# Optimization experiments

Measured on AMD Instinct MI355X. Metric: run time of the kernel, lower is better.

The kernel has to match this reference:

```python
import jax, jax.numpy as jnp
import numpy as np

HID = 512
VOCAB = 64
SAMPLE_PROB = 0.1


def lstm_cell(x, h, c, w_ih, w_hh, b_ih, b_hh):
    # PyTorch LSTMCell: gates ordered (i, f, g, o)
    gates = x @ w_ih.T + b_ih + h @ w_hh.T + b_hh
    i, f, g, o = jnp.split(gates, 4, axis=-1)
    i = jax.nn.sigmoid(i)
    f = jax.nn.sigmoid(f)
    g = jnp.tanh(g)
    o = jax.nn.sigmoid(o)
    c_new = f * c + i * g
    h_new = o * jnp.tanh(c_new)
    return h_new, c_new


def _linear_params(key, out_dim, in_dim):
    bound = 1.0 / np.sqrt(in_dim)
    kw, kb = jax.random.split(key)
    w = jax.random.uniform(kw, (out_dim, in_dim), jnp.float32, -bound, bound)
    b = jax.random.uniform(kb, (out_dim,), jnp.float32, -bound, bound)
    return w, b


def setup_inputs() -> dict:
    key = jax.random.key(0)
    ks = jax.random.split(key, 9)
    B, R, T = 128, 512, 128
    phi_w, phi_b = _linear_params(ks[0], HID, HID)          # decoder -> context
    psi_w, psi_b = _linear_params(ks[1], HID, HID)          # listener -> context
    w_ih0, b_ih0 = _linear_params(ks[2], 4 * HID, HID + VOCAB)
    w_hh0, b_hh0 = _linear_params(ks[3], 4 * HID, HID)
    w_ih1, b_ih1 = _linear_params(ks[4], 4 * HID, HID)
    w_hh1, b_hh1 = _linear_params(ks[5], 4 * HID, HID)
    out_w, out_b = _linear_params(ks[6], VOCAB, HID)
    h = jax.random.normal(ks[7], (B, R, HID), jnp.float32)
    y = jax.random.randint(ks[8], (B, T + 1), 0, VOCAB)
    return dict(h=h, phi_w=phi_w, phi_b=phi_b, psi_w=psi_w, psi_b=psi_b,
                w_ih0=w_ih0, w_hh0=w_hh0, b_ih0=b_ih0, b_hh0=b_hh0,
                w_ih1=w_ih1, w_hh1=w_hh1, b_ih1=b_ih1, b_hh1=b_hh1,
                out_w=out_w, out_b=out_b, y=y)


def reference(h, phi_w, phi_b, psi_w, psi_b,
              w_ih0, w_hh0, b_ih0, b_hh0,
              w_ih1, w_hh1, b_ih1, b_hh1,
              out_w, out_b, y):
    B = h.shape[0]
    T = y.shape[1] - 1
    # psi is applied to h identically every step; hoist it out of the loop.
    hp = h @ psi_w.T + psi_b                     # [B, R, HID]
    keys = jax.random.split(jax.random.key(42), T)
    z0 = y[:, 0]
    zeros = jnp.zeros((B, HID), h.dtype)
    carry0 = (zeros, zeros, zeros, zeros, z0)    # s0, cs0, s1, cs1, z

    def step(carry, xs):
        s0, cs0, s1, cs1, z = carry
        key, y_next = xs
        z_oh = jax.nn.one_hot(z, VOCAB, dtype=h.dtype)
        # additive-style attention context
        sq = s1 @ phi_w.T + phi_b                # [B, HID]
        e = jnp.einsum('bd,brd->br', sq, hp)     # [B, R]
        alpha = jax.nn.softmax(e, axis=1)
        c = jnp.einsum('br,brd->bd', alpha, hp)  # [B, HID]
        inp = jnp.concatenate([z_oh, c], axis=1)
        s0, cs0 = lstm_cell(inp, s0, cs0, w_ih0, w_hh0, b_ih0, b_hh0)
        s1, cs1 = lstm_cell(s0, s1, cs1, w_ih1, w_hh1, b_ih1, b_hh1)
        o = s1 @ out_w.T + out_b                 # [B, VOCAB]
        k1, k2 = jax.random.split(key)
        sampled = jax.random.categorical(k1, o, axis=1)
        do_sample = jax.random.bernoulli(k2, SAMPLE_PROB, (B,))
        z_next = jnp.where(do_sample, sampled, y_next)
        return (s0, cs0, s1, cs1, z_next), o

    xs = (keys, y[:, 1:].T)                      # per-step key, teacher token [T, B]
    _, outs = jax.lax.scan(step, carry0, xs)     # outs: [T, B, VOCAB]
    return jnp.transpose(outs, (1, 0, 2))        # [B, T, VOCAB]
```

## Files before the change

kernel.cpp:

```cpp
#include <hip/hip_runtime.h>
#include <math.h>


#define JAX_PARTITIONABLE 1

#define B_   128
#define HID_ 512
#define VOC_ 64
#define T_   128

#define S0_OFF    0u
#define CS0_OFF   65536u
#define S1_OFF    131072u
#define CS1_OFF   196608u
#define SQT_OFF   262144u
#define CPR_OFF   327680u
#define AMAT_OFF  393216u
#define W1PSI_OFF 655360u
#define BIAS0_OFF 1703936u
#define V_OFF     1705984u
#define PART_OFF  1706496u
#define GUM_OFF   5900800u
#define UB_OFF    6949376u
#define Z_OFF     6965760u

#define TF_TINY 1.17549435e-38f

__device__ __forceinline__ void tf2x32(unsigned k0, unsigned k1,
                                       unsigned& x0, unsigned& x1) {
  unsigned ks2 = k0 ^ k1 ^ 0x1BD11BDAu;
  const unsigned ks[3] = {k0, k1, ks2};
  const int rot0[4] = {13, 15, 26, 6};
  const int rot1[4] = {17, 29, 16, 24};
  x0 += ks[0]; x1 += ks[1];
  #pragma unroll
  for (int i = 0; i < 5; ++i) {
    #pragma unroll
    for (int r = 0; r < 4; ++r) {
      int rr = (i & 1) ? rot1[r] : rot0[r];
      x0 += x1;
      x1 = (x1 << rr) | (x1 >> (32 - rr));
      x1 ^= x0;
    }
    x0 += ks[(i + 1) % 3];
    x1 += ks[(i + 2) % 3] + (unsigned)(i + 1);
  }
}

__device__ __forceinline__ float bits_to_unit(unsigned bits) {
  return __uint_as_float((bits >> 9) | 0x3f800000u) - 1.0f;
}

__global__ __launch_bounds__(256) void k_random(const int* __restrict__ y,
                                                float* __restrict__ gum,
                                                float* __restrict__ ub,
                                                int* __restrict__ z) {
  int t = blockIdx.x, tid = threadIdx.x;
  unsigned ka, kb, k1a, k1b, k2a, k2b;
#if JAX_PARTITIONABLE
  ka = 0u; kb = (unsigned)t;
  tf2x32(0u, 42u, ka, kb);
  k1a = 0u; k1b = 0u; tf2x32(ka, kb, k1a, k1b);
  k2a = 0u; k2b = 1u; tf2x32(ka, kb, k2a, k2b);
  for (int j = tid; j < B_ * VOC_; j += 256) {
    unsigned x0 = 0u, x1 = (unsigned)j;
    tf2x32(k1a, k1b, x0, x1);
    unsigned bits = x0 ^ x1;
    float f = bits_to_unit(bits);
    float u = fmaxf(TF_TINY, f * (1.0f - TF_TINY) + TF_TINY);
    gum[(size_t)t * (B_ * VOC_) + j] = -logf(-logf(u));
  }
  if (tid < B_) {
    unsigned x0 = 0u, x1 = (unsigned)tid;
    tf2x32(k2a, k2b, x0, x1);
    ub[t * B_ + tid] = bits_to_unit(x0 ^ x1);
  }
#else
  {
    unsigned x0, x1, y0, y1;
    if (t < 64) {
      x0 = 2u * t;     x1 = 128u + 2u * t;     tf2x32(0u, 42u, x0, x1); ka = x0;
      y0 = 2u * t + 1; y1 = 128u + 2u * t + 1; tf2x32(0u, 42u, y0, y1); kb = y0;
    } else {
      x0 = 2u * t - 128u; x1 = 2u * t;         tf2x32(0u, 42u, x0, x1); ka = x1;
      y0 = 2u * t - 127u; y1 = 2u * t + 1;     tf2x32(0u, 42u, y0, y1); kb = y1;
    }
    unsigned e0a = 0u, e0b = 2u; tf2x32(ka, kb, e0a, e0b);
    unsigned e1a = 1u, e1b = 3u; tf2x32(ka, kb, e1a, e1b);
    k1a = e0a; k1b = e1a; k2a = e0b; k2b = e1b;
  }
  for (int j = tid; j < B_ * VOC_; j += 256) {
    unsigned x0, x1, bits;
    if (j < 4096) { x0 = (unsigned)j; x1 = (unsigned)(4096 + j); tf2x32(k1a, k1b, x0, x1); bits = x0; }
    else          { x0 = (unsigned)(j - 4096); x1 = (unsigned)j; tf2x32(k1a, k1b, x0, x1); bits = x1; }
    float f = bits_to_unit(bits);
    float u = fmaxf(TF_TINY, f * (1.0f - TF_TINY) + TF_TINY);
    gum[(size_t)t * (B_ * VOC_) + j] = -logf(-logf(u));
  }
  if (tid < B_) {
    unsigned x0, x1, bits;
    if (tid < 64) { x0 = (unsigned)tid; x1 = (unsigned)(64 + tid); tf2x32(k2a, k2b, x0, x1); bits = x0; }
    else          { x0 = (unsigned)(tid - 64); x1 = (unsigned)tid; tf2x32(k2a, k2b, x0, x1); bits = x1; }
    ub[t * B_ + tid] = bits_to_unit(bits);
  }
#endif
  if (t == 0 && tid < B_) z[tid] = y[tid * (T_ + 1)];
}

__global__ __launch_bounds__(256) void k_fold_misc(
    const float* __restrict__ psi_w, const float* __restrict__ phi_b,
    const float* __restrict__ w_ih0, const float* __restrict__ psi_b,
    const float* __restrict__ b_ih0, const float* __restrict__ b_hh0,
    float* __restrict__ vvec, float* __restrict__ bias0) {
  int gid = blockIdx.x * 256 + threadIdx.x;
  if (gid < 512) {
    float acc = 0.f;
    for (int j = 0; j < 512; ++j) acc += psi_w[j * 512 + gid] * phi_b[j];
    vvec[gid] = acc;
  } else if (gid < 512 + 2048) {
    int j = gid - 512;
    float acc = b_ih0[j] + b_hh0[j];
    const float* wr = w_ih0 + (size_t)j * 576 + 64;
    for (int d = 0; d < 512; ++d) acc += wr[d] * psi_b[d];
    bias0[j] = acc;
  }
}

__global__ __launch_bounds__(256) void k_gemm_tn(
    const float* __restrict__ A, const float* __restrict__ B, float* __restrict__ C,
    int K, int lda, int ldb, int ldc) {
  __shared__ float As[32][33], Bs[32][33];
  int n0 = blockIdx.x * 32, m0 = blockIdx.y * 32;
  int t = threadIdx.x, tx = t & 31, ty = t >> 5;
  float acc[4] = {0.f, 0.f, 0.f, 0.f};
  for (int k0 = 0; k0 < K; k0 += 32) {
    for (int l = t; l < 1024; l += 256) {
      int jj = l >> 5, mm = l & 31;
      As[jj][mm] = A[(size_t)(k0 + jj) * lda + m0 + mm];
      Bs[jj][mm] = B[(size_t)(k0 + jj) * ldb + n0 + mm];
    }
    __syncthreads();
    #pragma unroll 8
    for (int jj = 0; jj < 32; ++jj) {
      float bv = Bs[jj][tx];
      #pragma unroll
      for (int q = 0; q < 4; ++q) acc[q] += As[jj][ty + 8 * q] * bv;
    }
    __syncthreads();
  }
  #pragma unroll
  for (int q = 0; q < 4; ++q) C[(size_t)(m0 + ty + 8 * q) * ldc + n0 + tx] = acc[q];
}

__global__ __launch_bounds__(256) void k_gemm_nn(
    const float* __restrict__ A, const float* __restrict__ B, float* __restrict__ C,
    int K, int lda, int aoff, int ldb, int ldc) {
  __shared__ float As[32][33], Bs[32][33];
  int n0 = blockIdx.x * 32, m0 = blockIdx.y * 32;
  int t = threadIdx.x, tx = t & 31, ty = t >> 5;
  float acc[4] = {0.f, 0.f, 0.f, 0.f};
  for (int k0 = 0; k0 < K; k0 += 32) {
    for (int l = t; l < 1024; l += 256) {
      int r = l >> 5, c = l & 31;
      As[c][r] = A[(size_t)(m0 + r) * lda + aoff + k0 + c];
      Bs[r][c] = B[(size_t)(k0 + r) * ldb + n0 + c];
    }
    __syncthreads();
    #pragma unroll 8
    for (int kk = 0; kk < 32; ++kk) {
      float bv = Bs[kk][tx];
      #pragma unroll
      for (int q = 0; q < 4; ++q) acc[q] += As[kk][ty + 8 * q] * bv;
    }
    __syncthreads();
  }
  #pragma unroll
  for (int q = 0; q < 4; ++q) C[(size_t)(m0 + ty + 8 * q) * ldc + n0 + tx] = acc[q];
}

__global__ __launch_bounds__(256) void k_sqt_init(const float* __restrict__ vvec,
                                                  float* __restrict__ sqt) {
  int lin = blockIdx.x * 256 + threadIdx.x;
  if (lin < B_ * HID_) sqt[lin] = vvec[lin & 511];
}

__global__ __launch_bounds__(256) void k_attn(const float* __restrict__ h,
                                              const float* __restrict__ sqt,
                                              float* __restrict__ cpr) {
  __shared__ float hs[16 * 512];
  __shared__ float es[16];
  __shared__ float ps[16];
  int b = blockIdx.x, t = threadIdx.x;
  const float* hb = h + (size_t)b * 512 * 512;
  const float* sq = sqt + b * 512;
  int krow = t >> 4, g = t & 15;
  float m = -INFINITY, l = 0.f, a0 = 0.f, a1 = 0.f;
  int d0 = t, d1 = t + 256;
  for (int r0 = 0; r0 < 512; r0 += 16) {
    __syncthreads();
    const float* hr = hb + (size_t)(r0 + krow) * 512;
    float ep = 0.f;
    #pragma unroll
    for (int i = 0; i < 8; ++i) {
      int d = i * 64 + g * 4;
      float4 hv = *(const float4*)(hr + d);
      float4 sv = *(const float4*)(sq + d);
      ep += hv.x * sv.x + hv.y * sv.y + hv.z * sv.z + hv.w * sv.w;
      *(float4*)(&hs[krow * 512 + d]) = hv;
    }
    ep += __shfl_xor(ep, 1);
    ep += __shfl_xor(ep, 2);
    ep += __shfl_xor(ep, 4);
    ep += __shfl_xor(ep, 8);
    if (g == 0) es[krow] = ep;
    __syncthreads();
    float mc = es[0];
    #pragma unroll
    for (int k = 1; k < 16; ++k) mc = fmaxf(mc, es[k]);
    float mn = fmaxf(m, mc);
    if (t < 16) ps[t] = expf(es[t] - mn);
    __syncthreads();
    float sc = expf(m - mn);
    float ls = 0.f;
    float n0 = a0 * sc, n1 = a1 * sc;
    #pragma unroll
    for (int k = 0; k < 16; ++k) {
      float p = ps[k];
      ls += p;
      n0 += p * hs[k * 512 + d0];
      n1 += p * hs[k * 512 + d1];
    }
    m = mn; l = l * sc + ls; a0 = n0; a1 = n1;
  }
  cpr[b * 512 + d0] = a0 / l;
  cpr[b * 512 + d1] = a1 / l;
}

__global__ __launch_bounds__(256) void k_lstm_gemm(
    const float* __restrict__ X0, const float* __restrict__ W0,
    const float* __restrict__ X1, const float* __restrict__ W1,
    float* __restrict__ part) {
  __shared__ float Xs[16][128];
  __shared__ float Ws[16][64];
  int t = threadIdx.x;
  int jt = blockIdx.x * 64;
  int s = blockIdx.y;
  const float* X; const float* W; int kbase;
  if (s < 8) { X = X0; W = W0; kbase = s * 64; }
  else       { X = X1; W = W1; kbase = (s - 8) * 64; }
  float acc[8][4];
  #pragma unroll
  for (int i = 0; i < 8; ++i)
    #pragma unroll
    for (int q = 0; q < 4; ++q) acc[i][q] = 0.f;
  int b0 = (t & 15) * 8, j0 = (t >> 4) * 4;
  for (int kk = 0; kk < 64; kk += 16) {
    #pragma unroll
    for (int lo = 0; lo < 3; ++lo) {
      int u = t + lo * 256;
      if (u < 512) {
        int row = u >> 2;
        int kq = (u & 3) * 4;
        float4 xv = *(const float4*)(X + (size_t)row * 512 + kbase + kk + kq);
        Xs[kq + 0][row] = xv.x; Xs[kq + 1][row] = xv.y;
        Xs[kq + 2][row] = xv.z; Xs[kq + 3][row] = xv.w;
      } else {
        int w = u - 512;
        int row = w >> 2;
        int kq = (w & 3) * 4;
        float4 wv = *(const float4*)(W + (size_t)(jt + row) * 512 + kbase + kk + kq);
        Ws[kq + 0][row] = wv.x; Ws[kq + 1][row] = wv.y;
        Ws[kq + 2][row] = wv.z; Ws[kq + 3][row] = wv.w;
      }
    }
    __syncthreads();
    #pragma unroll
    for (int k = 0; k < 16; ++k) {
      float4 xa = *(const float4*)&Xs[k][b0];
      float4 xb = *(const float4*)&Xs[k][b0 + 4];
      float4 wa = *(const float4*)&Ws[k][j0];
      float xr[8] = {xa.x, xa.y, xa.z, xa.w, xb.x, xb.y, xb.z, xb.w};
      float wr[4] = {wa.x, wa.y, wa.z, wa.w};
      #pragma unroll
      for (int i = 0; i < 8; ++i)
        #pragma unroll
        for (int q = 0; q < 4; ++q) acc[i][q] += xr[i] * wr[q];
    }
    __syncthreads();
  }
  #pragma unroll
  for (int i = 0; i < 8; ++i) {
    float* pr = part + ((size_t)(s * 128 + b0 + i)) * 2048 + jt + j0;
    *(float4*)pr = make_float4(acc[i][0], acc[i][1], acc[i][2], acc[i][3]);
  }
}

__device__ __forceinline__ float sigm(float x) { return 1.0f / (1.0f + expf(-x)); }

__global__ __launch_bounds__(256) void k_lstm_cell(
    const float* __restrict__ part, const float* __restrict__ biasA,
    const float* __restrict__ bi, const float* __restrict__ bh,
    const float* __restrict__ woh, int ldoh,
    const int* __restrict__ z, float* __restrict__ s, float* __restrict__ cs) {
  int lin = blockIdx.x * 256 + threadIdx.x;
  int b = lin >> 9, d = lin & 511;
  int zb = woh ? z[b] : 0;
  float g4[4];
  #pragma unroll
  for (int g = 0; g < 4; ++g) {
    int j = g * 512 + d;
    float sum = biasA ? biasA[j] : (bi[j] + bh[j]);
    if (woh) sum += woh[(size_t)j * ldoh + zb];
    #pragma unroll
    for (int sl = 0; sl < 16; ++sl)
      sum += part[((size_t)(sl * 128 + b)) * 2048 + j];
    g4[g] = sum;
  }
  float ig = sigm(g4[0]), fg = sigm(g4[1]);
  float gg = tanhf(g4[2]), og = sigm(g4[3]);
  float cn = fg * cs[lin] + ig * gg;
  float sn = og * tanhf(cn);
  cs[lin] = cn;
  s[lin] = sn;
}

__global__ __launch_bounds__(512) void k_tail(
    int t, const float* __restrict__ part,
    const float* __restrict__ bi, const float* __restrict__ bh,
    const float* __restrict__ outw, const float* __restrict__ outb,
    const float* __restrict__ AmatT, const float* __restrict__ vvec,
    const float* __restrict__ gum, const float* __restrict__ ub,
    const int* __restrict__ y, const float* __restrict__ h,
    float* __restrict__ out, float* __restrict__ s1g, float* __restrict__ cs1,
    int* __restrict__ z, float* __restrict__ cpr) {
  __shared__ __align__(16) float hs[64 * 512];
  __shared__ __align__(16) float sl[512];
  __shared__ __align__(16) float sq[512];
  __shared__ float red[256];
  __shared__ float es_l[64];
  int b = blockIdx.x, tid = threadIdx.x;

  {
    int d = tid;
    int lin = b * 512 + d;
    float g4[4];
    #pragma unroll
    for (int g = 0; g < 4; ++g) {
      int j = g * 512 + d;
      float sum = bi[j] + bh[j];
      #pragma unroll
      for (int slc = 0; slc < 16; ++slc)
        sum += part[((size_t)(slc * 128 + b)) * 2048 + j];
      g4[g] = sum;
    }
    float ig = sigm(g4[0]), fg = sigm(g4[1]);
    float gg = tanhf(g4[2]), og = sigm(g4[3]);
    float cn = fg * cs1[lin] + ig * gg;
    float sn = og * tanhf(cn);
    cs1[lin] = cn;
    s1g[lin] = sn;
    sl[d] = sn;
  }
  __syncthreads();

  if (tid < 256) {
    int v = tid & 63, kg = tid >> 6;
    const float* wr = outw + (size_t)v * 512 + kg * 128;
    const float* sr = sl + kg * 128;
    float sum = 0.f;
    #pragma unroll 8
    for (int k = 0; k < 128; k += 4) {
      float4 w4 = *(const float4*)(wr + k);
      float4 s4 = *(const float4*)(sr + k);
      sum += w4.x * s4.x + w4.y * s4.y + w4.z * s4.z + w4.w * s4.w;
    }
    red[kg * 64 + v] = sum;
  }
  __syncthreads();
  if (tid < 64) {
    float o = red[tid] + red[64 + tid] + red[128 + tid] + red[192 + tid] + outb[tid];
    out[((size_t)b * T_ + t) * VOC_ + tid] = o;
    float val = o + gum[((size_t)t * B_ + b) * VOC_ + tid];
    int idx = tid;
    #pragma unroll
    for (int off = 1; off < 64; off <<= 1) {
      float ov = __shfl_xor(val, off);
      int oi = __shfl_xor(idx, off);
      if (ov > val || (ov == val && oi < idx)) { val = ov; idx = oi; }
    }
    if (tid == 0) {
      float u = ub[t * B_ + b];
      z[b] = (u < 0.1f) ? idx : y[b * (T_ + 1) + t + 1];
    }
  }

  {
    int d = tid;
    float av = vvec[d];
    const float* At = AmatT + d;
    for (int k = 0; k < 512; k += 4) {
      float p0 = At[(size_t)k * 512]       * sl[k];
      float p1 = At[(size_t)(k + 1) * 512] * sl[k + 1];
      float p2 = At[(size_t)(k + 2) * 512] * sl[k + 2];
      float p3 = At[(size_t)(k + 3) * 512] * sl[k + 3];
      av += p0 + p1 + p2 + p3;
    }
    sq[d] = av;
  }
  if (t == T_ - 1) return;
  __syncthreads();

  const float* hb = h + (size_t)b * (512 * 512);
  int krow = tid >> 4;
  int gq = tid & 15;
  int col = gq * 4;
  float4 sqr[8];
  #pragma unroll
  for (int i = 0; i < 8; ++i) sqr[i] = *(const float4*)(&sq[i * 64 + col]);

  float4 hv0[8], hv1[8];
  {
    const float* hr0 = hb + (size_t)krow * 512;
    const float* hr1 = hb + (size_t)(krow + 32) * 512;
    #pragma unroll
    for (int i = 0; i < 8; ++i) {
      hv0[i] = *(const float4*)(hr0 + i * 64 + col);
      hv1[i] = *(const float4*)(hr1 + i * 64 + col);
    }
    float ep0 = 0.f, ep1 = 0.f;
    #pragma unroll
    for (int i = 0; i < 8; ++i) {
      ep0 += hv0[i].x * sqr[i].x + hv0[i].y * sqr[i].y + hv0[i].z * sqr[i].z + hv0[i].w * sqr[i].w;
      *(float4*)(&hs[krow * 512 + i * 64 + col]) = hv0[i];
      ep1 += hv1[i].x * sqr[i].x + hv1[i].y * sqr[i].y + hv1[i].z * sqr[i].z + hv1[i].w * sqr[i].w;
      *(float4*)(&hs[(krow + 32) * 512 + i * 64 + col]) = hv1[i];
    }
    ep0 += __shfl_xor(ep0, 1); ep0 += __shfl_xor(ep0, 2);
    ep0 += __shfl_xor(ep0, 4); ep0 += __shfl_xor(ep0, 8);
    ep1 += __shfl_xor(ep1, 1); ep1 += __shfl_xor(ep1, 2);
    ep1 += __shfl_xor(ep1, 4); ep1 += __shfl_xor(ep1, 8);
    if (gq == 0) { es_l[krow] = ep0; es_l[krow + 32] = ep1; }
  }
  __syncthreads();

  float m = -INFINITY, l = 0.f, a0 = 0.f;
  int d0 = tid;
  int lane15 = tid & 15;
  for (int g = 0; g < 8; ++g) {
    if (g < 7) {
      const float* hr0 = hb + (size_t)((g + 1) * 64 + krow) * 512;
      const float* hr1 = hb + (size_t)((g + 1) * 64 + krow + 32) * 512;
      #pragma unroll
      for (int i = 0; i < 8; ++i) {
        hv0[i] = *(const float4*)(hr0 + i * 64 + col);
        hv1[i] = *(const float4*)(hr1 + i * 64 + col);
      }
    }
    #pragma unroll
    for (int lc = 0; lc < 4; ++lc) {
      float mc = es_l[lc * 16];
      #pragma unroll
      for (int k = 1; k < 16; ++k) mc = fmaxf(mc, es_l[lc * 16 + k]);
      float mn = fmaxf(m, mc);
      float pw = expf(es_l[lc * 16 + lane15] - mn);
      float sc = expf(m - mn);
      float ls = 0.f;
      float n0 = a0 * sc;
      #pragma unroll
      for (int k = 0; k < 16; ++k) {
        float p = __shfl(pw, k);
        ls += p;
        n0 += p * hs[(lc * 16 + k) * 512 + d0];
      }
      m = mn; l = l * sc + ls; a0 = n0;
    }
    __syncthreads();
    if (g < 7) {
      float ep0 = 0.f, ep1 = 0.f;
      #pragma unroll
      for (int i = 0; i < 8; ++i) {
        ep0 += hv0[i].x * sqr[i].x + hv0[i].y * sqr[i].y + hv0[i].z * sqr[i].z + hv0[i].w * sqr[i].w;
        *(float4*)(&hs[krow * 512 + i * 64 + col]) = hv0[i];
        ep1 += hv1[i].x * sqr[i].x + hv1[i].y * sqr[i].y + hv1[i].z * sqr[i].z + hv1[i].w * sqr[i].w;
        *(float4*)(&hs[(krow + 32) * 512 + i * 64 + col]) = hv1[i];
      }
      ep0 += __shfl_xor(ep0, 1); ep0 += __shfl_xor(ep0, 2);
      ep0 += __shfl_xor(ep0, 4); ep0 += __shfl_xor(ep0, 8);
      ep1 += __shfl_xor(ep1, 1); ep1 += __shfl_xor(ep1, 2);
      ep1 += __shfl_xor(ep1, 4); ep1 += __shfl_xor(ep1, 8);
      if (gq == 0) { es_l[krow] = ep0; es_l[krow + 32] = ep1; }
    }
    __syncthreads();
  }
  cpr[b * 512 + d0] = a0 / l;
}

extern "C" void kernel_launch(void* const* d_in, const int* in_sizes, int n_in,
                              void* d_out, int out_size, void* d_ws, size_t ws_size,
                              hipStream_t stream) {
  const float* h     = (const float*)d_in[0];
  const float* phi_w = (const float*)d_in[1];
  const float* phi_b = (const float*)d_in[2];
  const float* psi_w = (const float*)d_in[3];
  const float* psi_b = (const float*)d_in[4];
  const float* w_ih0 = (const float*)d_in[5];
  const float* w_hh0 = (const float*)d_in[6];
  const float* b_ih0 = (const float*)d_in[7];
  const float* b_hh0 = (const float*)d_in[8];
  const float* w_ih1 = (const float*)d_in[9];
  const float* w_hh1 = (const float*)d_in[10];
  const float* b_ih1 = (const float*)d_in[11];
  const float* b_hh1 = (const float*)d_in[12];
  const float* out_w = (const float*)d_in[13];
  const float* out_b = (const float*)d_in[14];
  const int*   y     = (const int*)d_in[15];

  float* out = (float*)d_out;
  float* ws  = (float*)d_ws;

  float* s0    = ws + S0_OFF;
  float* cs0   = ws + CS0_OFF;
  float* s1    = ws + S1_OFF;
  float* cs1   = ws + CS1_OFF;
  float* sqt   = ws + SQT_OFF;
  float* cpr   = ws + CPR_OFF;
  float* AmatT = ws + AMAT_OFF;
  float* W1psi = ws + W1PSI_OFF;
  float* bias0 = ws + BIAS0_OFF;
  float* vvec  = ws + V_OFF;
  float* part  = ws + PART_OFF;
  float* gum   = ws + GUM_OFF;
  float* ub    = ws + UB_OFF;
  int*   z     = (int*)(ws + Z_OFF);

  hipMemsetAsync(s0, 0, 4 * (size_t)B_ * HID_ * sizeof(float), stream);

  k_random<<<T_, 256, 0, stream>>>(y, gum, ub, z);
  k_fold_misc<<<10, 256, 0, stream>>>(psi_w, phi_b, w_ih0, psi_b, b_ih0, b_hh0, vvec, bias0);
  k_gemm_tn<<<dim3(16, 16), 256, 0, stream>>>(phi_w, psi_w, AmatT, 512, 512, 512, 512);
  k_gemm_nn<<<dim3(16, 64), 256, 0, stream>>>(w_ih0, psi_w, W1psi, 512, 576, 64, 512, 512);
  k_sqt_init<<<256, 256, 0, stream>>>(vvec, sqt);
  k_attn<<<128, 256, 0, stream>>>(h, sqt, cpr);

  for (int t = 0; t < T_; ++t) {
    k_lstm_gemm<<<dim3(32, 16), 256, 0, stream>>>(cpr, W1psi, s0, w_hh0, part);
    k_lstm_cell<<<256, 256, 0, stream>>>(part, bias0, nullptr, nullptr, w_ih0, 576, z, s0, cs0);
    k_lstm_gemm<<<dim3(32, 16), 256, 0, stream>>>(s0, w_ih1, s1, w_hh1, part);
    k_tail<<<128, 512, 0, stream>>>(t, part, b_ih1, b_hh1, out_w, out_b, AmatT, vvec,
                                    gum, ub, y, h, out, s1, cs1, z, cpr);
  }
}
```

Measured before the change: 12.72 ms.

## Fuse LSTM gate GEMM with cell update using ping-pong state buffers

Result: slower. 18.46 ms (+45.1%).

```diff
diff --git a/kernel.cpp b/kernel.cpp
--- a/kernel.cpp
+++ b/kernel.cpp
@@ -184,6 +184,15 @@
   if (lin < B_ * HID_) sqt[lin] = vvec[lin & 511];
 }
 
+__global__ __launch_bounds__(256) void k_transpose_ow(const float* __restrict__ outw,
+                                                      float* __restrict__ outwT) {
+  int gid = blockIdx.x * 256 + threadIdx.x;
+  if (gid < 512 * 64) {
+    int k = gid >> 6, v = gid & 63;
+    outwT[gid] = outw[(size_t)v * 512 + k];
+  }
+}
+
 __global__ __launch_bounds__(256) void k_attn(const float* __restrict__ h,
                                               const float* __restrict__ sqt,
                                               float* __restrict__ cpr) {
@@ -236,103 +245,85 @@
   cpr[b * 512 + d1] = a1 / l;
 }
 
-__global__ __launch_bounds__(256) void k_lstm_gemm(
+__device__ __forceinline__ float sigm(float x) { return 1.0f / (1.0f + expf(-x)); }
+
+__global__ __launch_bounds__(256) void k_fused(
     const float* __restrict__ X0, const float* __restrict__ W0,
     const float* __restrict__ X1, const float* __restrict__ W1,
-    float* __restrict__ part) {
-  __shared__ float Xs[16][128];
-  __shared__ float Ws[16][64];
-  int t = threadIdx.x;
-  int jt = blockIdx.x * 64;
-  int s = blockIdx.y;
-  const float* X; const float* W; int kbase;
-  if (s < 8) { X = X0; W = W0; kbase = s * 64; }
-  else       { X = X1; W = W1; kbase = (s - 8) * 64; }
-  float acc[8][4];
+    const float* __restrict__ biasA, const float* __restrict__ bi,
+    const float* __restrict__ bh, const float* __restrict__ woh, int ldoh,
+    const int* __restrict__ z, float* __restrict__ snew, float* __restrict__ cs) {
+  __shared__ float Xs[64][16];
+  __shared__ float Ws[64][64];
+  __shared__ float tot[16][64];
+  int tid = threadIdx.x;
+  int dt0 = blockIdx.x * 16, bt0 = blockIdx.y * 16;
+  int b = tid & 15, j0 = (tid >> 4) * 4;
+  float total[4];
+  int zb = woh ? z[bt0 + b] : 0;
   #pragma unroll
-  for (int i = 0; i < 8; ++i)
-    #pragma unroll
-    for (int q = 0; q < 4; ++q) acc[i][q] = 0.f;
-  int b0 = (t & 15) * 8, j0 = (t >> 4) * 4;
-  for (int kk = 0; kk < 64; kk += 16) {
-    #pragma unroll
-    for (int lo = 0; lo < 3; ++lo) {
-      int u = t + lo * 256;
-      if (u < 512) {
-        int row = u >> 2;
-        int kq = (u & 3) * 4;
-        float4 xv = *(const float4*)(X + (size_t)row * 512 + kbase + kk + kq);
-        Xs[kq + 0][row] = xv.x; Xs[kq + 1][row] = xv.y;
-        Xs[kq + 2][row] = xv.z; Xs[kq + 3][row] = xv.w;
-      } else {
-        int w = u - 512;
-        int row = w >> 2;
-        int kq = (w & 3) * 4;
-        float4 wv = *(const float4*)(W + (size_t)(jt + row) * 512 + kbase + kk + kq);
-        Ws[kq + 0][row] = wv.x; Ws[kq + 1][row] = wv.y;
-        Ws[kq + 2][row] = wv.z; Ws[kq + 3][row] = wv.w;
+  for (int q = 0; q < 4; ++q) {
+    int jl = j0 + q;
+    int jg = (jl >> 4) * 512 + dt0 + (jl & 15);
+    float tq = biasA ? biasA[jg] : (bi[jg] + bh[jg]);
+    if (woh) tq += woh[(size_t)jg * ldoh + zb];
+    total[q] = tq;
+  }
+  for (int s = 0; s < 16; ++s) {
+    const float* X = (s < 8) ? X0 : X1;
+    const float* W = (s < 8) ? W0 : W1;
+    int kb = (s & 7) * 64;
+    __syncthreads();
+    {
+      int xb = tid >> 4, xk = (tid & 15) * 4;
+      float4 xv = *(const float4*)(X + (size_t)(bt0 + xb) * 512 + kb + xk);
+      Xs[xk + 0][xb] = xv.x; Xs[xk + 1][xb] = xv.y;
+      Xs[xk + 2][xb] = xv.z; Xs[xk + 3][xb] = xv.w;
+      #pragma unroll
+      for (int r = 0; r < 4; ++r) {
+        int wi = tid + r * 256;
+        int wj = wi >> 4, wk = (wi & 15) * 4;
+        int jg = (wj >> 4) * 512 + dt0 + (wj & 15);
+        float4 wv = *(const float4*)(W + (size_t)jg * 512 + kb + wk);
+        Ws[wk + 0][wj] = wv.x; Ws[wk + 1][wj] = wv.y;
+        Ws[wk + 2][wj] = wv.z; Ws[wk + 3][wj] = wv.w;
       }
     }
     __syncthreads();
-    #pragma unroll
-    for (int k = 0; k < 16; ++k) {
-      float4 xa = *(const float4*)&Xs[k][b0];
-      float4 xb = *(const float4*)&Xs[k][b0 + 4];
-      float4 wa = *(const float4*)&Ws[k][j0];
-      float xr[8] = {xa.x, xa.y, xa.z, xa.w, xb.x, xb.y, xb.z, xb.w};
-      float wr[4] = {wa.x, wa.y, wa.z, wa.w};
-      #pragma unroll
-      for (int i = 0; i < 8; ++i)
-        #pragma unroll
-        for (int q = 0; q < 4; ++q) acc[i][q] += xr[i] * wr[q];
-    }
-    __syncthreads();
+    float p0 = 0.f, p1 = 0.f, p2 = 0.f, p3 = 0.f;
+    #pragma unroll
+    for (int k = 0; k < 64; ++k) {
+      float xv = Xs[k][b];
+      float4 w4 = *(const float4*)&Ws[k][j0];
+      p0 += xv * w4.x; p1 += xv * w4.y; p2 += xv * w4.z; p3 += xv * w4.w;
+    }
+    total[0] += p0; total[1] += p1; total[2] += p2; total[3] += p3;
   }
   #pragma unroll
-  for (int i = 0; i < 8; ++i) {
-    float* pr = part + ((size_t)(s * 128 + b0 + i)) * 2048 + jt + j0;
-    *(float4*)pr = make_float4(acc[i][0], acc[i][1], acc[i][2], acc[i][3]);
-  }
-}
-
-__device__ __forceinline__ float sigm(float x) { return 1.0f / (1.0f + expf(-x)); }
-
-__global__ __launch_bounds__(256) void k_lstm_cell(
-    const float* __restrict__ part, const float* __restrict__ biasA,
-    const float* __restrict__ bi, const float* __restrict__ bh,
-    const float* __restrict__ woh, int ldoh,
-    const int* __restrict__ z, float* __restrict__ s, float* __restrict__ cs) {
-  int lin = blockIdx.x * 256 + threadIdx.x;
-  int b = lin >> 9, d = lin & 511;
-  int zb = woh ? z[b] : 0;
-  float g4[4];
-  #pragma unroll
-  for (int g = 0; g < 4; ++g) {
-    int j = g * 512 + d;
-    float sum = biasA ? biasA[j] : (bi[j] + bh[j]);
-    if (woh) sum += woh[(size_t)j * ldoh + zb];
-    #pragma unroll
-    for (int sl = 0; sl < 16; ++sl)
-      sum += part[((size_t)(sl * 128 + b)) * 2048 + j];
-    g4[g] = sum;
-  }
-  float ig = sigm(g4[0]), fg = sigm(g4[1]);
-  float gg = tanhf(g4[2]), og = sigm(g4[3]);
-  float cn = fg * cs[lin] + ig * gg;
-  float sn = og * tanhf(cn);
-  cs[lin] = cn;
-  s[lin] = sn;
-}
-
-__global__ __launch_bounds__(512) void k_tail(
-    int t, const float* __restrict__ part,
-    const float* __restrict__ bi, const float* __restrict__ bh,
-    const float* __restrict__ outw, const float* __restrict__ outb,
+  for (int q = 0; q < 4; ++q) tot[b][j0 + q] = total[q];
+  __syncthreads();
+  {
+    int b2 = tid & 15, dl = tid >> 4;
+    int lin = (bt0 + b2) * 512 + dt0 + dl;
+    float g4[4];
+    #pragma unroll
+    for (int g = 0; g < 4; ++g) g4[g] = tot[b2][g * 16 + dl];
+    float ig = sigm(g4[0]), fg = sigm(g4[1]);
+    float gg = tanhf(g4[2]), og = sigm(g4[3]);
+    float cn = fg * cs[lin] + ig * gg;
+    float sn = og * tanhf(cn);
+    cs[lin] = cn;
+    snew[lin] = sn;
+  }
+}
+
+__global__ __launch_bounds__(512) void k_tail2(
+    int t, const float* __restrict__ s1n,
+    const float* __restrict__ outwT, const float* __restrict__ outb,
     const float* __restrict__ AmatT, const float* __restrict__ vvec,
     const float* __restrict__ gum, const float* __restrict__ ub,
     const int* __restrict__ y, const float* __restrict__ h,
-    float* __restrict__ out, float* __restrict__ s1g, float* __restrict__ cs1,
-    int* __restrict__ z, float* __restrict__ cpr) {
+    float* __restrict__ out, int* __restrict__ z, float* __restrict__ cpr) {
   __shared__ __align__(16) float hs[64 * 512];
   __shared__ __align__(16) float sl[512];
   __shared__ __align__(16) float sq[512];
@@ -340,39 +331,20 @@
   __shared__ float es_l[64];
   int b = blockIdx.x, tid = threadIdx.x;
 
-  {
-    int d = tid;
-    int lin = b * 512 + d;
-    float g4[4];
-    #pragma unroll
-    for (int g = 0; g < 4; ++g) {
-      int j = g * 512 + d;
-      float sum = bi[j] + bh[j];
-      #pragma unroll
-      for (int slc = 0; slc < 16; ++slc)
-        sum += part[((size_t)(slc * 128 + b)) * 2048 + j];
-      g4[g] = sum;
-    }
-    float ig = sigm(g4[0]), fg = sigm(g4[1]);
-    float gg = tanhf(g4[2]), og = sigm(g4[3]);
-    float cn = fg * cs1[lin] + ig * gg;
-    float sn = og * tanhf(cn);
-    cs1[lin] = cn;
-    s1g[lin] = sn;
-    sl[d] = sn;
-  }
+  sl[tid] = s1n[b * 512 + tid];
   __syncthreads();
 
   if (tid < 256) {
     int v = tid & 63, kg = tid >> 6;
-    const float* wr = outw + (size_t)v * 512 + kg * 128;
-    const float* sr = sl + kg * 128;
     float sum = 0.f;
     #pragma unroll 8
     for (int k = 0; k < 128; k += 4) {
-      float4 w4 = *(const float4*)(wr + k);
-      float4 s4 = *(const float4*)(sr + k);
-      sum += w4.x * s4.x + w4.y * s4.y + w4.z * s4.z + w4.w * s4.w;
+      int kk = kg * 128 + k;
+      float q0 = outwT[(size_t)(kk + 0) * 64 + v] * sl[kk + 0];
+      float q1 = outwT[(size_t)(kk + 1) * 64 + v] * sl[kk + 1];
+      float q2 = outwT[(size_t)(kk + 2) * 64 + v] * sl[kk + 2];
+      float q3 = outwT[(size_t)(kk + 3) * 64 + v] * sl[kk + 3];
+      sum += q0 + q1 + q2 + q3;
     }
     red[kg * 64 + v] = sum;
   }
@@ -518,9 +490,9 @@
   float* out = (float*)d_out;
   float* ws  = (float*)d_ws;
 
-  float* s0    = ws + S0_OFF;
+  float* s0A   = ws + S0_OFF;
   float* cs0   = ws + CS0_OFF;
-  float* s1    = ws + S1_OFF;
+  float* s1A   = ws + S1_OFF;
   float* cs1   = ws + CS1_OFF;
   float* sqt   = ws + SQT_OFF;
   float* cpr   = ws + CPR_OFF;
@@ -528,25 +500,34 @@
   float* W1psi = ws + W1PSI_OFF;
   float* bias0 = ws + BIAS0_OFF;
   float* vvec  = ws + V_OFF;
-  float* part  = ws + PART_OFF;
+  float* s0B   = ws + PART_OFF;
+  float* s1B   = ws + PART_OFF + 65536;
+  float* outwT = ws + PART_OFF + 131072;
   float* gum   = ws + GUM_OFF;
   float* ub    = ws + UB_OFF;
   int*   z     = (int*)(ws + Z_OFF);
 
-  hipMemsetAsync(s0, 0, 4 * (size_t)B_ * HID_ * sizeof(float), stream);
+  hipMemsetAsync(s0A, 0, 4 * (size_t)B_ * HID_ * sizeof(float), stream);
 
   k_random<<<T_, 256, 0, stream>>>(y, gum, ub, z);
   k_fold_misc<<<10, 256, 0, stream>>>(psi_w, phi_b, w_ih0, psi_b, b_ih0, b_hh0, vvec, bias0);
   k_gemm_tn<<<dim3(16, 16), 256, 0, stream>>>(phi_w, psi_w, AmatT, 512, 512, 512, 512);
   k_gemm_nn<<<dim3(16, 64), 256, 0, stream>>>(w_ih0, psi_w, W1psi, 512, 576, 64, 512, 512);
+  k_transpose_ow<<<128, 256, 0, stream>>>(out_w, outwT);
   k_sqt_init<<<256, 256, 0, stream>>>(vvec, sqt);
   k_attn<<<128, 256, 0, stream>>>(h, sqt, cpr);
 
   for (int t = 0; t < T_; ++t) {
-    k_lstm_gemm<<<dim3(32, 16), 256, 0, stream>>>(cpr, W1psi, s0, w_hh0, part);
-    k_lstm_cell<<<256, 256, 0, stream>>>(part, bias0, nullptr, nullptr, w_ih0, 576, z, s0, cs0);
-    k_lstm_gemm<<<dim3(32, 16), 256, 0, stream>>>(s0, w_ih1, s1, w_hh1, part);
-    k_tail<<<128, 512, 0, stream>>>(t, part, b_ih1, b_hh1, out_w, out_b, AmatT, vvec,
-                                    gum, ub, y, h, out, s1, cs1, z, cpr);
-  }
-}
+    int rd = t & 1;
+    float* s0r = rd ? s0B : s0A; float* s0w = rd ? s0A : s0B;
+    float* s1r = rd ? s1B : s1A; float* s1w = rd ? s1A : s1B;
+    k_fused<<<dim3(32, 8), 256, 0, stream>>>(cpr, W1psi, s0r, w_hh0,
+                                             bias0, nullptr, nullptr, w_ih0, 576,
+                                             z, s0w, cs0);
+    k_fused<<<dim3(32, 8), 256, 0, stream>>>(s0w, w_ih1, s1r, w_hh1,
+                                             nullptr, b_ih1, b_hh1, nullptr, 0,
+                                             z, s1w, cs1);
+    k_tail2<<<128, 512, 0, stream>>>(t, s1w, outwT, out_b, AmatT, vvec,
+                                     gum, ub, y, h, out, z, cpr);
+  }
+}
```
